# Kernel optimization log

Hardware: AMD Instinct MI355X
Metric: run time of the kernel (lower is better)

## Reference

```python
import jax, jax.numpy as jnp
import numpy as np
import itertools

B, G, FEAT, IMG = 2048, 8, 512, 1024
SCALES = list(range(G, 1, -1))  # [8,7,6,5,4,3,2]
SUBSAMPLE = 12


def setup_inputs() -> dict:
    key = jax.random.key(0)
    keys = jax.random.split(key, 1 + 2 * len(SCALES))
    rng = np.random.default_rng(0)
    inp = {"input": jax.random.normal(keys[0], (B, G, FEAT), dtype=jnp.float32)}
    for i, scale in enumerate(SCALES):
        perms = np.array(list(itertools.permutations(range(G), scale)), dtype=np.int32)
        n_sub = min(SUBSAMPLE, len(perms))
        sel = rng.choice(len(perms), n_sub, replace=False)
        inp[f"perms{i}"] = jnp.asarray(perms[sel])  # [n_sub, scale] int32
        lim = 1.0 / np.sqrt(scale * FEAT)
        inp[f"W{i}"] = jax.random.uniform(keys[1 + 2 * i], (IMG, scale * FEAT), minval=-lim, maxval=lim, dtype=jnp.float32)
        inp[f"b{i}"] = jax.random.uniform(keys[2 + 2 * i], (IMG,), minval=-lim, maxval=lim, dtype=jnp.float32)
    return inp


def _forward(input, perms_list, W_list, b_list):
    outs = []
    for perms, W, b in zip(perms_list, W_list, b_list):
        # gather: [B, n_sub, scale, FEAT] -> [B, n_sub, scale*FEAT]
        g = input[:, perms, :]
        g = g.reshape(g.shape[0], g.shape[1], -1)
        # batched linear over all subsamples, then mean over subsamples
        y = jnp.einsum('bsf,df->bsd', g, W) + b  # [B, n_sub, IMG]
        outs.append(y.mean(axis=1))
    return jnp.concatenate(outs, axis=1)  # [B, len(SCALES)*IMG]


def reference(input, perms0, W0, b0, perms1, W1, b1, perms2, W2, b2,
              perms3, W3, b3, perms4, W4, b4, perms5, W5, b5, perms6, W6, b6):
    perms_list = [perms0, perms1, perms2, perms3, perms4, perms5, perms6]
    W_list = [W0, W1, W2, W3, W4, W5, W6]
    b_list = [b0, b1, b2, b3, b4, b5, b6]
    return _forward(input, perms_list, W_list, b_list)
```

## Files before the change

kernel.cpp:

```cpp
#include <hip/hip_runtime.h>

typedef unsigned short u16;
typedef __bf16 bf16x8 __attribute__((ext_vector_type(8)));
typedef float f32x4 __attribute__((ext_vector_type(4)));

__device__ __forceinline__ u16 f2bf(float f) {
  unsigned int u = __float_as_uint(f);
  return (u16)((u + 0x7fffu + ((u >> 16) & 1u)) >> 16);
}


__global__ __launch_bounds__(256) void k_prep(
    const float* __restrict__ x,
    const int* p0, const int* p1, const int* p2, const int* p3,
    const int* p4, const int* p5, const int* p6,
    const float* W0, const float* W1, const float* W2, const float* W3,
    const float* W4, const float* W5, const float* W6,
    u16* __restrict__ Xb16, u16* __restrict__ Wtil) {
  __shared__ float sC[64];
  const int bid = blockIdx.x;
  const int t = threadIdx.x;
  if (bid < 1792) {
    const int r0 = bid << 2;
    const int i = r0 >> 10;
    const int scale = 8 - i;
    const int K = scale << 9;
    const int d0 = r0 - (i << 10);
    if (t < 64) {
      const int g = t >> 3, j = t & 7;
      float v = 0.f;
      if (j < scale) {
        const int* p = (i == 0) ? p0 : (i == 1) ? p1 : (i == 2) ? p2 :
                       (i == 3) ? p3 : (i == 4) ? p4 : (i == 5) ? p5 : p6;
        int cnt = 0;
        for (int s = 0; s < 12; ++s) cnt += (p[s * scale + j] == g) ? 1 : 0;
        v = (float)cnt * (1.0f / 12.0f);
      }
      sC[t] = v;
    }
    __syncthreads();
    const float* Wi = (i == 0) ? W0 : (i == 1) ? W1 : (i == 2) ? W2 :
                      (i == 3) ? W3 : (i == 4) ? W4 : (i == 5) ? W5 : W6;
    const int u = t & 63;
    const int gq = t >> 6;
    u16* dst = Wtil + ((size_t)r0 << 12);
    for (int r = 0; r < 4; ++r) {
      const float* wrow = Wi + (size_t)(d0 + r) * K;
      float a0[8], a1[8];
#pragma unroll
      for (int e = 0; e < 8; ++e) { a0[e] = 0.f; a1[e] = 0.f; }
      for (int j = 0; j < scale; ++j) {
        const float* wp = wrow + j * 512 + (u << 3);
        const float4 wa = *reinterpret_cast<const float4*>(wp);
        const float4 wb = *reinterpret_cast<const float4*>(wp + 4);
        const float c0 = sC[(gq << 4) + j];
        const float c1 = sC[(gq << 4) + 8 + j];
        a0[0] += c0 * wa.x; a0[1] += c0 * wa.y; a0[2] += c0 * wa.z; a0[3] += c0 * wa.w;
        a0[4] += c0 * wb.x; a0[5] += c0 * wb.y; a0[6] += c0 * wb.z; a0[7] += c0 * wb.w;
        a1[0] += c1 * wa.x; a1[1] += c1 * wa.y; a1[2] += c1 * wa.z; a1[3] += c1 * wa.w;
        a1[4] += c1 * wb.x; a1[5] += c1 * wb.y; a1[6] += c1 * wb.z; a1[7] += c1 * wb.w;
      }
      uint4 o0, o1;
      o0.x = (unsigned)f2bf(a0[0]) | ((unsigned)f2bf(a0[1]) << 16);
      o0.y = (unsigned)f2bf(a0[2]) | ((unsigned)f2bf(a0[3]) << 16);
      o0.z = (unsigned)f2bf(a0[4]) | ((unsigned)f2bf(a0[5]) << 16);
      o0.w = (unsigned)f2bf(a0[6]) | ((unsigned)f2bf(a0[7]) << 16);
      o1.x = (unsigned)f2bf(a1[0]) | ((unsigned)f2bf(a1[1]) << 16);
      o1.y = (unsigned)f2bf(a1[2]) | ((unsigned)f2bf(a1[3]) << 16);
      o1.z = (unsigned)f2bf(a1[4]) | ((unsigned)f2bf(a1[5]) << 16);
      o1.w = (unsigned)f2bf(a1[6]) | ((unsigned)f2bf(a1[7]) << 16);
      u16* drow = dst + ((size_t)r << 12) + (gq << 10) + (u << 3);
      *reinterpret_cast<uint4*>(drow) = o0;
      *reinterpret_cast<uint4*>(drow + 512) = o1;
    }
  } else {
    const int tid0 = ((bid - 1792) << 8) | t;
    const float4* X4 = reinterpret_cast<const float4*>(x);
    uint4* O = reinterpret_cast<uint4*>(Xb16);
#pragma unroll 4
    for (int it = 0; it < 16; ++it) {
      const int e = tid0 + (it << 16);
      const float4 a = X4[(size_t)e * 2];
      const float4 c = X4[(size_t)e * 2 + 1];
      uint4 o;
      o.x = (unsigned)f2bf(a.x) | ((unsigned)f2bf(a.y) << 16);
      o.y = (unsigned)f2bf(a.z) | ((unsigned)f2bf(a.w) << 16);
      o.z = (unsigned)f2bf(c.x) | ((unsigned)f2bf(c.y) << 16);
      o.w = (unsigned)f2bf(c.z) | ((unsigned)f2bf(c.w) << 16);
      O[e] = o;
    }
  }
}

__device__ __forceinline__ void gl_lds16(const u16* g, u16* l) {
  __builtin_amdgcn_global_load_lds(
      (const __attribute__((address_space(1))) void*)g,
      (__attribute__((address_space(3))) void*)l, 16, 0, 0);
}

#define WAIT_VM8 0x0F78
#define WAIT_VM0 0x0F70

__global__ __launch_bounds__(256) void k_gemm(
    const u16* __restrict__ A, const u16* __restrict__ Bm,
    const float* b0, const float* b1, const float* b2, const float* b3,
    const float* b4, const float* b5, const float* b6,
    float* __restrict__ out) {
  __shared__ u16 lds[2 * 16384];
  const int bid = blockIdx.x;
  const int xcd = bid & 7;
  const int sid = bid >> 3;
  const int m0 = (sid & 15) * 128;
  const int n0 = (xcd * 7 + (sid >> 4)) * 128;

  const int tid = threadIdx.x;
  const int lane = tid & 63;
  const int wave = tid >> 6;
  const int quad = lane >> 4;
  const int l15 = lane & 15;
  const int waveM = (wave >> 1) * 64;
  const int waveN = (wave & 1) * 64;

  const int srow = tid >> 3;
  const int sslot = tid & 7;
  const int gch = (sslot - srow) & 7;
  const u16* pA0 = A + (size_t)(m0 + srow) * 4096 + gch * 8;
  const u16* pB0 = Bm + (size_t)(n0 + srow) * 4096 + gch * 8;
  const size_t strideR = (size_t)32 * 4096;
  u16* lA0 = lds + tid * 8;
  u16* lB0 = lds + 8192 + tid * 8;

  int offA[2][4], offB[2][4];
#pragma unroll
  for (int tt = 0; tt < 2; ++tt) {
#pragma unroll
    for (int q = 0; q < 4; ++q) {
      int rowA = waveM + q * 16 + l15;
      offA[tt][q] = rowA * 64 + (((tt * 4 + quad) + rowA) & 7) * 8;
      int rowB = waveN + q * 16 + l15;
      offB[tt][q] = 8192 + rowB * 64 + (((tt * 4 + quad) + rowB) & 7) * 8;
    }
  }

  f32x4 acc[4][4];
#pragma unroll
  for (int q = 0; q < 4; ++q)
#pragma unroll
    for (int c = 0; c < 4; ++c) {
      f32x4 z = {0.f, 0.f, 0.f, 0.f};
      acc[q][c] = z;
    }

#pragma unroll
  for (int j = 0; j < 4; ++j) {
    gl_lds16(pA0 + j * strideR, lA0 + j * 2048);
    gl_lds16(pB0 + j * strideR, lB0 + j * 2048);
  }

  for (int kt = 0; kt < 63; ++kt) {
    const size_t ko = (size_t)(kt + 1) * 64;
    const int nb = ((kt + 1) & 1) << 14;
#pragma unroll
    for (int j = 0; j < 4; ++j) {
      gl_lds16(pA0 + j * strideR + ko, lA0 + nb + j * 2048);
      gl_lds16(pB0 + j * strideR + ko, lB0 + nb + j * 2048);
    }
    __builtin_amdgcn_s_waitcnt(WAIT_VM8);
    __builtin_amdgcn_s_barrier();
    const int boff = (kt & 1) << 14;
#pragma unroll
    for (int tt = 0; tt < 2; ++tt) {
      bf16x8 av[4], bv[4];
#pragma unroll
      for (int q = 0; q < 4; ++q) av[q] = *reinterpret_cast<const bf16x8*>(lds + boff + offA[tt][q]);
#pragma unroll
      for (int c = 0; c < 4; ++c) bv[c] = *reinterpret_cast<const bf16x8*>(lds + boff + offB[tt][c]);
#pragma unroll
      for (int q = 0; q < 4; ++q)
#pragma unroll
        for (int c = 0; c < 4; ++c)
          acc[q][c] = __builtin_amdgcn_mfma_f32_16x16x32_bf16(av[q], bv[c], acc[q][c], 0, 0, 0);
    }
    __builtin_amdgcn_s_barrier();
  }

  __builtin_amdgcn_s_waitcnt(WAIT_VM0);
  __builtin_amdgcn_s_barrier();
  {
    const int boff = 1 << 14;
#pragma unroll
    for (int tt = 0; tt < 2; ++tt) {
      bf16x8 av[4], bv[4];
#pragma unroll
      for (int q = 0; q < 4; ++q) av[q] = *reinterpret_cast<const bf16x8*>(lds + boff + offA[tt][q]);
#pragma unroll
      for (int c = 0; c < 4; ++c) bv[c] = *reinterpret_cast<const bf16x8*>(lds + boff + offB[tt][c]);
#pragma unroll
      for (int q = 0; q < 4; ++q)
#pragma unroll
        for (int c = 0; c < 4; ++c)
          acc[q][c] = __builtin_amdgcn_mfma_f32_16x16x32_bf16(av[q], bv[c], acc[q][c], 0, 0, 0);
    }
  }

  const int isc = n0 >> 10;
  const float* bi = (isc == 0) ? b0 : (isc == 1) ? b1 : (isc == 2) ? b2 :
                    (isc == 3) ? b3 : (isc == 4) ? b4 : (isc == 5) ? b5 : b6;
#pragma unroll
  for (int c = 0; c < 4; ++c) {
    const int ncol = n0 + waveN + c * 16 + l15;
    const float bias = bi[ncol & 1023];
#pragma unroll
    for (int q = 0; q < 4; ++q) {
      const int mbase = m0 + waveM + q * 16 + quad * 4;
#pragma unroll
      for (int reg = 0; reg < 4; ++reg)
        out[(size_t)(mbase + reg) * 7168 + ncol] = acc[q][c][reg] + bias;
    }
  }
}

extern "C" void kernel_launch(void* const* d_in, const int* in_sizes, int n_in,
                              void* d_out, int out_size, void* d_ws, size_t ws_size,
                              hipStream_t stream) {
  const float* input = (const float*)d_in[0];
  const int* perms[7];
  const float* W[7];
  const float* bias[7];
  for (int i = 0; i < 7; ++i) {
    perms[i] = (const int*)d_in[1 + 3 * i];
    W[i]     = (const float*)d_in[2 + 3 * i];
    bias[i]  = (const float*)d_in[3 + 3 * i];
  }
  char* ws = (char*)d_ws;
  u16* Xb16 = (u16*)ws;
  u16* Wtil = (u16*)(ws + (size_t)2048 * 4096 * 2);

  k_prep<<<2048, 256, 0, stream>>>(input,
                                   perms[0], perms[1], perms[2], perms[3],
                                   perms[4], perms[5], perms[6],
                                   W[0], W[1], W[2], W[3], W[4], W[5], W[6],
                                   Xb16, Wtil);
  k_gemm<<<896, 256, 0, stream>>>(Xb16, Wtil,
                                  bias[0], bias[1], bias[2], bias[3],
                                  bias[4], bias[5], bias[6],
                                  (float*)d_out);
}
```

Before: 325.7 us.

## Rewrite GEMM as 256x256 tile, 8-wave ping-pong pipeline with split stages

Replaces the 128x128 four-wave double-buffered GEMM with 256x256 block tiles computed by eight waves in a 2x4 layout. Each K-tile load is split into half-tile stages interleaved with MFMA groups, using barriers and s_setprio so memory traffic overlaps tensor-core work. The grid shrinks from 896 blocks to 224, one per 256x256 output tile. This raises data reuse per block and hides load latency, at the cost of fewer blocks than compute units, heavier register use (a 32-entry accumulator per wave) and 128KB of LDS.

```diff
diff --git a/kernel.cpp b/kernel.cpp
--- a/kernel.cpp
+++ b/kernel.cpp
@@ -98,124 +98,185 @@
       (__attribute__((address_space(3))) void*)l, 16, 0, 0);
 }
 
-#define WAIT_VM8 0x0F78
-#define WAIT_VM0 0x0F70
-
-__global__ __launch_bounds__(256) void k_gemm(
+#define WAIT_VM2   0x0F72
+#define WAIT_VM0   0x0F70
+#define WAIT_LGKM0 0xC07F
+
+#define MFMA_Q(MB, NB, AV, BV)                                               \
+  _Pragma("unroll")                                                          \
+  for (int q_ = 0; q_ < 4; ++q_) {                                           \
+    _Pragma("unroll")                                                        \
+    for (int n_ = 0; n_ < 2; ++n_) {                                         \
+      acc[(MB) + q_][(NB) + n_] = __builtin_amdgcn_mfma_f32_16x16x32_bf16(   \
+          AV[q_][0], BV[n_][0], acc[(MB) + q_][(NB) + n_], 0, 0, 0);         \
+      acc[(MB) + q_][(NB) + n_] = __builtin_amdgcn_mfma_f32_16x16x32_bf16(   \
+          AV[q_][1], BV[n_][1], acc[(MB) + q_][(NB) + n_], 0, 0, 0);         \
+    }                                                                        \
+  }
+
+#define RD_A4(DB, QB)                                                        \
+  _Pragma("unroll")                                                          \
+  for (int q_ = 0; q_ < 4; ++q_) {                                           \
+    aR[q_][0] = *reinterpret_cast<const bf16x8*>(lds + (DB) + offA[(QB) + q_]);         \
+    aR[q_][1] = *reinterpret_cast<const bf16x8*>(lds + (DB) + (offA[(QB) + q_] ^ 32));  \
+  }
+
+#define RD_B2(DB, ARR, FB)                                                   \
+  _Pragma("unroll")                                                          \
+  for (int n_ = 0; n_ < 2; ++n_) {                                           \
+    ARR[n_][0] = *reinterpret_cast<const bf16x8*>(lds + (DB) + offB[(FB) + n_]);        \
+    ARR[n_][1] = *reinterpret_cast<const bf16x8*>(lds + (DB) + (offB[(FB) + n_] ^ 32)); \
+  }
+
+__global__ __launch_bounds__(512, 2) void k_gemm(
     const u16* __restrict__ A, const u16* __restrict__ Bm,
     const float* b0, const float* b1, const float* b2, const float* b3,
     const float* b4, const float* b5, const float* b6,
     float* __restrict__ out) {
-  __shared__ u16 lds[2 * 16384];
+  __shared__ u16 lds[65536];
   const int bid = blockIdx.x;
-  const int xcd = bid & 7;
-  const int sid = bid >> 3;
-  const int m0 = (sid & 15) * 128;
-  const int n0 = (xcd * 7 + (sid >> 4)) * 128;
+  const int blockM = (bid & 7) * 256;
+  const int blockN = (bid >> 3) * 256;
 
   const int tid = threadIdx.x;
   const int lane = tid & 63;
-  const int wave = tid >> 6;
+  const int wid = tid >> 6;
+  const int wr = wid >> 2;
+  const int wc = wid & 3;
   const int quad = lane >> 4;
   const int l15 = lane & 15;
-  const int waveM = (wave >> 1) * 64;
-  const int waveN = (wave & 1) * 64;
 
   const int srow = tid >> 3;
   const int sslot = tid & 7;
   const int gch = (sslot - srow) & 7;
-  const u16* pA0 = A + (size_t)(m0 + srow) * 4096 + gch * 8;
-  const u16* pB0 = Bm + (size_t)(n0 + srow) * 4096 + gch * 8;
-  const size_t strideR = (size_t)32 * 4096;
-  u16* lA0 = lds + tid * 8;
-  u16* lB0 = lds + 8192 + tid * 8;
-
-  int offA[2][4], offB[2][4];
-#pragma unroll
-  for (int tt = 0; tt < 2; ++tt) {
-#pragma unroll
-    for (int q = 0; q < 4; ++q) {
-      int rowA = waveM + q * 16 + l15;
-      offA[tt][q] = rowA * 64 + (((tt * 4 + quad) + rowA) & 7) * 8;
-      int rowB = waveN + q * 16 + l15;
-      offB[tt][q] = 8192 + rowB * 64 + (((tt * 4 + quad) + rowB) & 7) * 8;
-    }
-  }
-
-  f32x4 acc[4][4];
-#pragma unroll
-  for (int q = 0; q < 4; ++q)
-#pragma unroll
-    for (int c = 0; c < 4; ++c) {
+  const u16* gA0 = A + (size_t)(blockM + srow) * 4096 + gch * 8;
+  const u16* gB0 = Bm + (size_t)(blockN + srow) * 4096 + gch * 8;
+
+  int offA[8], offB[4];
+#pragma unroll
+  for (int q = 0; q < 8; ++q) {
+    const int r = q * 16 + l15;
+    offA[q] = wr * 8192 + r * 64 + ((quad + r) & 7) * 8;
+  }
+#pragma unroll
+  for (int f = 0; f < 4; ++f) {
+    const int r = (wc & 1) * 64 + f * 16 + l15;
+    offB[f] = 16384 + (wc >> 1) * 8192 + r * 64 + ((quad + r) & 7) * 8;
+  }
+
+  f32x4 acc[8][4];
+#pragma unroll
+  for (int m = 0; m < 8; ++m)
+#pragma unroll
+    for (int n = 0; n < 4; ++n) {
       f32x4 z = {0.f, 0.f, 0.f, 0.f};
-      acc[q][c] = z;
-    }
-
-#pragma unroll
-  for (int j = 0; j < 4; ++j) {
-    gl_lds16(pA0 + j * strideR, lA0 + j * 2048);
-    gl_lds16(pB0 + j * strideR, lB0 + j * 2048);
-  }
-
-  for (int kt = 0; kt < 63; ++kt) {
-    const size_t ko = (size_t)(kt + 1) * 64;
-    const int nb = ((kt + 1) & 1) << 14;
-#pragma unroll
-    for (int j = 0; j < 4; ++j) {
-      gl_lds16(pA0 + j * strideR + ko, lA0 + nb + j * 2048);
-      gl_lds16(pB0 + j * strideR + ko, lB0 + nb + j * 2048);
-    }
-    __builtin_amdgcn_s_waitcnt(WAIT_VM8);
-    __builtin_amdgcn_s_barrier();
-    const int boff = (kt & 1) << 14;
-#pragma unroll
-    for (int tt = 0; tt < 2; ++tt) {
-      bf16x8 av[4], bv[4];
-#pragma unroll
-      for (int q = 0; q < 4; ++q) av[q] = *reinterpret_cast<const bf16x8*>(lds + boff + offA[tt][q]);
-#pragma unroll
-      for (int c = 0; c < 4; ++c) bv[c] = *reinterpret_cast<const bf16x8*>(lds + boff + offB[tt][c]);
-#pragma unroll
-      for (int q = 0; q < 4; ++q)
-#pragma unroll
-        for (int c = 0; c < 4; ++c)
-          acc[q][c] = __builtin_amdgcn_mfma_f32_16x16x32_bf16(av[q], bv[c], acc[q][c], 0, 0, 0);
-    }
-    __builtin_amdgcn_s_barrier();
-  }
-
+      acc[m][n] = z;
+    }
+
+  auto stage = [&](int mat, int h, int t, int db) {
+    const u16* g = (mat ? gB0 : gA0) + (size_t)h * (128 * 4096) + (size_t)t * 64;
+    u16* l = lds + db + mat * 16384 + h * 8192 + (tid << 3);
+    gl_lds16(g, l);
+    gl_lds16(g + (size_t)(64 * 4096), l + 4096);
+  };
+
+  stage(0, 0, 0, 0); stage(0, 1, 0, 0); stage(1, 0, 0, 0); stage(1, 1, 0, 0);
+  stage(0, 0, 1, 32768);
+  __builtin_amdgcn_s_waitcnt(WAIT_VM2);
+  __builtin_amdgcn_s_barrier();
+
+  bf16x8 aR[4][2], bL[2][2], bH[2][2];
+
+  for (int j = 0; j < 32; ++j) {
+    const int t1 = 2 * j + 1;
+    const int t2 = (j < 31) ? 2 * j + 2 : 63;
+    const int t3 = (j < 31) ? 2 * j + 3 : 63;
+
+    RD_A4(0, 0) RD_B2(0, bL, 0)
+    stage(0, 1, t1, 32768);
+    __builtin_amdgcn_s_barrier();
+    __builtin_amdgcn_s_waitcnt(WAIT_LGKM0);
+    __builtin_amdgcn_s_setprio(1);
+    MFMA_Q(0, 0, aR, bL)
+    __builtin_amdgcn_s_setprio(0);
+    __builtin_amdgcn_s_barrier();
+
+    RD_B2(0, bH, 2)
+    stage(1, 0, t1, 32768);
+    __builtin_amdgcn_s_barrier();
+    __builtin_amdgcn_s_waitcnt(WAIT_LGKM0);
+    __builtin_amdgcn_s_setprio(1);
+    MFMA_Q(0, 2, aR, bH)
+    __builtin_amdgcn_s_setprio(0);
+    __builtin_amdgcn_s_barrier();
+
+    RD_A4(0, 4)
+    stage(1, 1, t1, 32768);
+    __builtin_amdgcn_s_barrier();
+    __builtin_amdgcn_s_waitcnt(WAIT_LGKM0);
+    __builtin_amdgcn_s_setprio(1);
+    MFMA_Q(4, 2, aR, bH)
+    __builtin_amdgcn_s_setprio(0);
+    __builtin_amdgcn_s_barrier();
+
+    stage(0, 0, t2, 0);
+    __builtin_amdgcn_s_barrier();
+    __builtin_amdgcn_s_setprio(1);
+    MFMA_Q(4, 0, aR, bL)
+    __builtin_amdgcn_s_setprio(0);
+    __builtin_amdgcn_s_waitcnt(WAIT_VM2);
+    __builtin_amdgcn_s_barrier();
+
+    RD_A4(32768, 0) RD_B2(32768, bL, 0)
+    stage(0, 1, t2, 0);
+    __builtin_amdgcn_s_barrier();
+    __builtin_amdgcn_s_waitcnt(WAIT_LGKM0);
+    __builtin_amdgcn_s_setprio(1);
+    MFMA_Q(0, 0, aR, bL)
+    __builtin_amdgcn_s_setprio(0);
+    __builtin_amdgcn_s_barrier();
+
+    RD_B2(32768, bH, 2)
+    stage(1, 0, t2, 0);
+    __builtin_amdgcn_s_barrier();
+    __builtin_amdgcn_s_waitcnt(WAIT_LGKM0);
+    __builtin_amdgcn_s_setprio(1);
+    MFMA_Q(0, 2, aR, bH)
+    __builtin_amdgcn_s_setprio(0);
+    __builtin_amdgcn_s_barrier();
+
+    RD_A4(32768, 4)
+    stage(1, 1, t2, 0);
+    __builtin_amdgcn_s_barrier();
+    __builtin_amdgcn_s_waitcnt(WAIT_LGKM0);
+    __builtin_amdgcn_s_setprio(1);
+    MFMA_Q(4, 2, aR, bH)
+    __builtin_amdgcn_s_setprio(0);
+    __builtin_amdgcn_s_barrier();
+
+    stage(0, 0, t3, 32768);
+    __builtin_amdgcn_s_barrier();
+    __builtin_amdgcn_s_setprio(1);
+    MFMA_Q(4, 0, aR, bL)
+    __builtin_amdgcn_s_setprio(0);
+    __builtin_amdgcn_s_waitcnt(WAIT_VM2);
+    __builtin_amdgcn_s_barrier();
+  }
   __builtin_amdgcn_s_waitcnt(WAIT_VM0);
-  __builtin_amdgcn_s_barrier();
-  {
-    const int boff = 1 << 14;
-#pragma unroll
-    for (int tt = 0; tt < 2; ++tt) {
-      bf16x8 av[4], bv[4];
-#pragma unroll
-      for (int q = 0; q < 4; ++q) av[q] = *reinterpret_cast<const bf16x8*>(lds + boff + offA[tt][q]);
-#pragma unroll
-      for (int c = 0; c < 4; ++c) bv[c] = *reinterpret_cast<const bf16x8*>(lds + boff + offB[tt][c]);
-#pragma unroll
-      for (int q = 0; q < 4; ++q)
-#pragma unroll
-        for (int c = 0; c < 4; ++c)
-          acc[q][c] = __builtin_amdgcn_mfma_f32_16x16x32_bf16(av[q], bv[c], acc[q][c], 0, 0, 0);
-    }
-  }
-
-  const int isc = n0 >> 10;
+
+  const int isc = blockN >> 10;
   const float* bi = (isc == 0) ? b0 : (isc == 1) ? b1 : (isc == 2) ? b2 :
                     (isc == 3) ? b3 : (isc == 4) ? b4 : (isc == 5) ? b5 : b6;
 #pragma unroll
-  for (int c = 0; c < 4; ++c) {
-    const int ncol = n0 + waveN + c * 16 + l15;
+  for (int nf = 0; nf < 4; ++nf) {
+    const int ncol = blockN + wc * 64 + nf * 16 + l15;
     const float bias = bi[ncol & 1023];
 #pragma unroll
-    for (int q = 0; q < 4; ++q) {
-      const int mbase = m0 + waveM + q * 16 + quad * 4;
+    for (int mq = 0; mq < 8; ++mq) {
+      const int mbase = blockM + wr * 128 + mq * 16 + quad * 4;
 #pragma unroll
       for (int reg = 0; reg < 4; ++reg)
-        out[(size_t)(mbase + reg) * 7168 + ncol] = acc[q][c][reg] + bias;
+        out[(size_t)(mbase + reg) * 7168 + ncol] = acc[mq][nf][reg] + bias;
     }
   }
 }
@@ -241,7 +302,7 @@
                                    perms[4], perms[5], perms[6],
                                    W[0], W[1], W[2], W[3], W[4], W[5], W[6],
                                    Xb16, Wtil);
-  k_gemm<<<896, 256, 0, stream>>>(Xb16, Wtil,
+  k_gemm<<<224, 512, 0, stream>>>(Xb16, Wtil,
                                   bias[0], bias[1], bias[2], bias[3],
                                   bias[4], bias[5], bias[6],
                                   (float*)d_out);
```

Result: faster. 303.4 us (-6.8%).
